# Kernel optimization log

Hardware: AMD Instinct MI355X
Metric: run time of the kernel (lower is better)

The kernel has to match this reference:

```python
import jax, jax.numpy as jnp
import numpy as np

NUM_NODES = 100000
NUM_EDGES = 1600000
NUM_GRAPHS = 64
D_IN = 128
HID = 256
N_ATTR = 8
D_OUT = 1


def setup_inputs() -> dict:
    key = jax.random.key(0)
    ks = jax.random.split(key, 16)
    x = jax.random.normal(ks[0], (NUM_NODES, D_IN), dtype=jnp.float32)
    edge_index = jax.random.randint(ks[1], (2, NUM_EDGES), 0, NUM_NODES, dtype=jnp.int64)
    batch = jnp.sort(jax.random.randint(ks[2], (NUM_NODES,), 0, NUM_GRAPHS, dtype=jnp.int64))
    graph_attr = jax.random.normal(ks[3], (NUM_GRAPHS, N_ATTR), dtype=jnp.float32)
    def lin(k, fi, fo):
        s = 1.0 / np.sqrt(fi)
        return jax.random.uniform(k, (fi, fo), jnp.float32, -s, s)
    # SAGEConv: lin_l (applied to aggregated neighbors, has bias) + lin_r (root, no bias)
    W1l = lin(ks[4], D_IN, HID); b1 = jnp.zeros((HID,), jnp.float32)
    W1r = lin(ks[5], D_IN, HID)
    W2l = lin(ks[6], HID, HID); b2 = jnp.zeros((HID,), jnp.float32)
    W2r = lin(ks[7], HID, HID)
    Wf1 = lin(ks[8], HID + N_ATTR, HID); bf1 = jnp.zeros((HID,), jnp.float32)
    Wf2 = lin(ks[9], HID, D_OUT); bf2 = jnp.zeros((D_OUT,), jnp.float32)
    return {"x": x, "edge_index": edge_index, "batch": batch, "graph_attr": graph_attr,
            "W1l": W1l, "b1": b1, "W1r": W1r, "W2l": W2l, "b2": b2, "W2r": W2r,
            "Wf1": Wf1, "bf1": bf1, "Wf2": Wf2, "bf2": bf2}


def _mean_agg(h, src, dst, num_segments):
    # gather source features, scatter-mean into destination nodes
    s = jax.ops.segment_sum(h[src], dst, num_segments=num_segments)
    cnt = jax.ops.segment_sum(jnp.ones((src.shape[0], 1), h.dtype), dst, num_segments=num_segments)
    return s / jnp.maximum(cnt, 1.0)


def _sage(h, src, dst, Wl, b, Wr):
    agg = _mean_agg(h, src, dst, h.shape[0])
    return agg @ Wl + b + h @ Wr


def reference(x, edge_index, batch, graph_attr, W1l, b1, W1r, W2l, b2, W2r, Wf1, bf1, Wf2, bf2):
    src, dst = edge_index[0], edge_index[1]
    h = jax.nn.relu(_sage(x, src, dst, W1l, b1, W1r))
    h = _sage(h, src, dst, W2l, b2, W2r)
    # global mean pool over graphs
    gsum = jax.ops.segment_sum(h, batch, num_segments=NUM_GRAPHS)
    gcnt = jax.ops.segment_sum(jnp.ones((h.shape[0], 1), h.dtype), batch, num_segments=NUM_GRAPHS)
    g = gsum / jnp.maximum(gcnt, 1.0)
    g = jnp.concatenate([g, graph_attr.reshape(-1, N_ATTR)], axis=1)
    g = jax.nn.relu(g @ Wf1 + bf1)
    return g @ Wf2 + bf2
```

## Files before the change

### kernel.cpp

```cpp
#include <hip/hip_runtime.h>
#include <stdint.h>

#define NN 100000
#define NE 1600000
#define NG 64
#define DIN 128
#define HID 256
#define NATTR 8
#define NBK 391
#define CAP 6144
#define PCH 4096
#define BWW 25000
#define CB 12756
#define AEL 2048

typedef unsigned short u16;
typedef __attribute__((ext_vector_type(8))) short s16x8;
typedef __attribute__((ext_vector_type(4))) float f32x4;
typedef __attribute__((ext_vector_type(2))) float f32x2;

__device__ __forceinline__ int imaxi(int a, int b) { return a > b ? a : b; }
__device__ __forceinline__ u16 f2bf(float f) {
    unsigned u = __float_as_uint(f);
    return (u16)((u + 0x7fffu + ((u >> 16) & 1u)) >> 16);
}
__device__ __forceinline__ void gload16(const void* g, void* l) {
    __builtin_amdgcn_global_load_lds((const __attribute__((address_space(1))) void*)g,
                                     (__attribute__((address_space(3))) void*)l, 16, 0, 0);
}


__global__ void k_prep(const float4* __restrict__ x4, ushort4* __restrict__ xb4,
                       const float* __restrict__ W1l, const float* __restrict__ W1r,
                       u16* __restrict__ W1lt, u16* __restrict__ W1rt,
                       float4* __restrict__ P84, const int* __restrict__ batch,
                       int* __restrict__ goff, int* __restrict__ gcnt,
                       int* __restrict__ cursor) {
    int b = blockIdx.x, t = threadIdx.x;
    if (b < CB) {
        int i = b * 256 + t;
        const int NX4 = NN * DIN / 4;
        if (i < NX4) {
            float4 v = x4[i];
            ushort4 o;
            o.x = f2bf(v.x); o.y = f2bf(v.y); o.z = f2bf(v.z); o.w = f2bf(v.w);
            xb4[i] = o;
        } else {
            int j = i - NX4;
            if (j < 32768) {
                int n = j >> 7, k = j & 127;
                W1lt[j] = f2bf(W1l[k * HID + n]);
            } else if (j < 65536) {
                int jj = j - 32768;
                int n = jj >> 7, k = jj & 127;
                W1rt[jj] = f2bf(W1r[k * HID + n]);
            }
        }
    } else if (b < CB + 256) {
        int i = (b - CB) * 256 + t;
        P84[i] = make_float4(0.f, 0.f, 0.f, 0.f);
    } else {
        for (int i = t; i < NBK; i += 256) cursor[i] = 0;
        int g = t;
        if (g <= NG) {
            int lo = 0, hi = NN;
            while (lo < hi) {
                int mid = (lo + hi) >> 1;
                if (batch[mid] < g) lo = mid + 1; else hi = mid;
            }
            goff[g] = lo;
        }
        __syncthreads();
        if (g < NG) gcnt[g] = goff[g + 1] - goff[g];
    }
}


__global__ __launch_bounds__(256) void k_part(const int* __restrict__ ei,
                                              int* __restrict__ cursor,
                                              unsigned* __restrict__ pairs) {
    __shared__ unsigned spk[PCH];
    __shared__ unsigned short sbk[PCH];
    __shared__ int hist[NBK], gb[NBK];
    __shared__ int sc[512];
    int t = threadIdx.x;
    int c0 = blockIdx.x * PCH;
    int n = NE - c0; if (n > PCH) n = PCH;
    for (int i = t; i < NBK; i += 256) hist[i] = 0;
    __syncthreads();
    unsigned mypk[16]; unsigned short mybk[16]; int myoff[16];
#pragma unroll
    for (int j = 0; j < 16; j++) {
        int i = t + j * 256;
        myoff[j] = -1;
        if (i < n) {
            int e = c0 + i;
            unsigned d = (unsigned)__builtin_nontemporal_load(&ei[NE + e]);
            unsigned s = (unsigned)__builtin_nontemporal_load(&ei[e]);
            unsigned bk = d >> 8;
            mypk[j] = ((d & 255u) << 24) | s;
            mybk[j] = (unsigned short)bk;
            myoff[j] = atomicAdd(&hist[bk], 1);
        }
    }
    __syncthreads();
    sc[t] = (t < NBK) ? hist[t] : 0;
    sc[t + 256] = (t + 256 < NBK) ? hist[t + 256] : 0;
    __syncthreads();
    for (int off = 1; off < 512; off <<= 1) {
        int v0 = (t >= off) ? sc[t - off] : 0;
        int v1 = (t + 256 >= off) ? sc[t + 256 - off] : 0;
        __syncthreads();
        sc[t] += v0; sc[t + 256] += v1;
        __syncthreads();
    }
    if (t < NBK && hist[t] > 0) gb[t] = atomicAdd(&cursor[t], hist[t]);
    if (t + 256 < NBK && hist[t + 256] > 0)
        gb[t + 256] = atomicAdd(&cursor[t + 256], hist[t + 256]);
    __syncthreads();
#pragma unroll
    for (int j = 0; j < 16; j++) {
        if (myoff[j] >= 0) {
            int bk = mybk[j];
            int pos = sc[bk] - hist[bk] + myoff[j];
            spk[pos] = mypk[j];
            sbk[pos] = (unsigned short)bk;
        }
    }
    __syncthreads();
    for (int i = t; i < n; i += 256) {
        int bk = sbk[i];
        int local = gb[bk] + (i - (sc[bk] - hist[bk]));
        pairs[(size_t)bk * CAP + local] = spk[i];
    }
}


__global__ __launch_bounds__(256) void k_csr(const unsigned* __restrict__ pairs,
                                             const int* __restrict__ cursor,
                                             int* __restrict__ rowptr,
                                             unsigned* __restrict__ col) {
    __shared__ unsigned colL[CAP];
    __shared__ int csc[512];
    __shared__ int cnt[256], cur[256], sc[256];
    int b = blockIdx.x, t = threadIdx.x;
    csc[t] = (t < NBK) ? cursor[t] : 0;
    csc[t + 256] = (t + 256 < NBK) ? cursor[t + 256] : 0;
    __syncthreads();
    for (int off = 1; off < 512; off <<= 1) {
        int v0 = (t >= off) ? csc[t - off] : 0;
        int v1 = (t + 256 >= off) ? csc[t + 256 - off] : 0;
        __syncthreads();
        csc[t] += v0; csc[t + 256] += v1;
        __syncthreads();
    }
    int obase = (b == 0) ? 0 : csc[b - 1];
    int ecnt = cursor[b];
    const unsigned* pp = pairs + (size_t)b * CAP;
    cnt[t] = 0;
    __syncthreads();
    for (int i = t; i < ecnt; i += 256)
        atomicAdd(&cnt[pp[i] >> 24], 1);
    __syncthreads();
    sc[t] = cnt[t];
    __syncthreads();
    for (int off = 1; off < 256; off <<= 1) {
        int v = (t >= off) ? sc[t - off] : 0;
        __syncthreads();
        sc[t] += v;
        __syncthreads();
    }
    int lr = sc[t] - cnt[t];
    cur[t] = lr;
    int node = (b << 8) + t;
    if (node < NN) rowptr[node] = obase + lr;
    if (b == NBK - 1 && t == 0) rowptr[NN] = obase + ecnt;
    __syncthreads();
    for (int i = t; i < ecnt; i += 256) {
        unsigned p = pp[i];
        int dl = p >> 24;
        int pos = atomicAdd(&cur[dl], 1);
        int dd = cnt[dl]; if (dd > 32767) dd = 32767;
        colL[pos] = ((unsigned)dd << 17) | (p & 0xFFFFFFu);
    }
    __syncthreads();
    for (int i = t; i < ecnt; i += 256)
        col[obase + i] = colL[i];
}


__global__ __launch_bounds__(256, 8) void k_agg(const uint4* __restrict__ xb4,
                                                uint4* __restrict__ agg4,
                                                const int* __restrict__ rowptr,
                                                const unsigned* __restrict__ col) {
    __shared__ unsigned scol[AEL];
    int t = threadIdx.x;
    int base = blockIdx.x * 16;
    int wave = t >> 6, lane = t & 63;
    int qtr = lane >> 4, li = lane & 15;
    int node = base + (wave << 2) + qtr;
    int s = rowptr[node], e = rowptr[node + 1];
    int bs = rowptr[base], be = rowptr[base + 16];
    int bn = be - bs;
    bool inl = bn <= AEL;
    if (inl)
        for (int j = t; j < bn; j += 256) scol[j] = col[bs + j];
    __syncthreads();

    f32x2 b01 = {0.f, 0.f}, b23 = {0.f, 0.f}, b45 = {0.f, 0.f}, b67 = {0.f, 0.f};
    const uint4* xp = xb4 + li;

#define ACC8(V) do { \
        f32x2 p; \
        p[0] = __uint_as_float((V).x << 16); p[1] = __uint_as_float((V).x & 0xffff0000u); b01 += p; \
        p[0] = __uint_as_float((V).y << 16); p[1] = __uint_as_float((V).y & 0xffff0000u); b23 += p; \
        p[0] = __uint_as_float((V).z << 16); p[1] = __uint_as_float((V).z & 0xffff0000u); b45 += p; \
        p[0] = __uint_as_float((V).w << 16); p[1] = __uint_as_float((V).w & 0xffff0000u); b67 += p; \
    } while (0)

#define CL(X) scol[(X) - bs]
#define CG(X) col[X]
#define AGG_BODY(CIDX) do { \
        for (; i + 8 <= e; i += 8) { \
            unsigned c0 = (CIDX(i + 0)) & 0x1FFFFu; \
            unsigned c1 = (CIDX(i + 1)) & 0x1FFFFu; \
            unsigned c2 = (CIDX(i + 2)) & 0x1FFFFu; \
            unsigned c3 = (CIDX(i + 3)) & 0x1FFFFu; \
            unsigned c4 = (CIDX(i + 4)) & 0x1FFFFu; \
            unsigned c5 = (CIDX(i + 5)) & 0x1FFFFu; \
            unsigned c6 = (CIDX(i + 6)) & 0x1FFFFu; \
            unsigned c7 = (CIDX(i + 7)) & 0x1FFFFu; \
            uint4 w0 = xp[(size_t)c0 * 16]; \
            uint4 w1 = xp[(size_t)c1 * 16]; \
            uint4 w2 = xp[(size_t)c2 * 16]; \
            uint4 w3 = xp[(size_t)c3 * 16]; \
            uint4 w4 = xp[(size_t)c4 * 16]; \
            uint4 w5 = xp[(size_t)c5 * 16]; \
            uint4 w6 = xp[(size_t)c6 * 16]; \
            uint4 w7 = xp[(size_t)c7 * 16]; \
            ACC8(w0); ACC8(w1); ACC8(w2); ACC8(w3); \
            ACC8(w4); ACC8(w5); ACC8(w6); ACC8(w7); \
        } \
        for (; i + 2 <= e; i += 2) { \
            unsigned c0 = (CIDX(i + 0)) & 0x1FFFFu; \
            unsigned c1 = (CIDX(i + 1)) & 0x1FFFFu; \
            uint4 w0 = xp[(size_t)c0 * 16]; \
            uint4 w1 = xp[(size_t)c1 * 16]; \
            ACC8(w0); ACC8(w1); \
        } \
        if (i < e) { \
            unsigned c0 = (CIDX(i)) & 0x1FFFFu; \
            uint4 w0 = xp[(size_t)c0 * 16]; \
            ACC8(w0); \
        } \
    } while (0)

    int i = s;
    if (inl) { AGG_BODY(CL); } else { AGG_BODY(CG); }
#undef AGG_BODY
#undef CL
#undef CG
#undef ACC8

    float inv = 1.f / (float)imaxi(e - s, 1);
    uint4 o;
    o.x = (((unsigned)f2bf(b01[1] * inv)) << 16) | (unsigned)f2bf(b01[0] * inv);
    o.y = (((unsigned)f2bf(b23[1] * inv)) << 16) | (unsigned)f2bf(b23[0] * inv);
    o.z = (((unsigned)f2bf(b45[1] * inv)) << 16) | (unsigned)f2bf(b45[0] * inv);
    o.w = (((unsigned)f2bf(b67[1] * inv)) << 16) | (unsigned)f2bf(b67[0] * inv);
    agg4[(size_t)node * 16 + li] = o;
}


__global__ __launch_bounds__(512) void k_gemm1(
    const u16* __restrict__ agg1, const u16* __restrict__ xb,
    const u16* __restrict__ W1lt, const u16* __restrict__ W1rt,
    const float* __restrict__ b1, u16* __restrict__ h1t) {
    __shared__ u16 As[128][32];
    __shared__ u16 Bs[256][32];
    int t = threadIdx.x;
    int m0 = blockIdx.x * 128;
    int wave = t >> 6, lane = t & 63;
    int wm = wave & 1, wn = wave >> 1;
    int lm = lane & 15, quad = lane >> 4;
    int ar = t >> 2, aq = t & 3;
    f32x4 acc[4][4] = {};
    const u16* Ap = agg1;
    const u16* Bp = W1lt;
#pragma unroll
    for (int ph = 0; ph < 2; ph++) {
        for (int k0 = 0; k0 < DIN; k0 += 32) {
            gload16(Ap + (size_t)(m0 + ar) * DIN + k0 + aq * 8, &As[wave * 16][0]);
#pragma unroll
            for (int i = 0; i < 2; i++) {
                int r = (t + i * 512) >> 2;
                gload16(Bp + (size_t)r * DIN + k0 + aq * 8, &Bs[wave * 16 + i * 128][0]);
            }
            __syncthreads();
            s16x8 af[4], bfr[4];
#pragma unroll
            for (int i = 0; i < 4; i++) {
                af[i]  = *(const s16x8*)&As[wm * 64 + i * 16 + lm][quad * 8];
                bfr[i] = *(const s16x8*)&Bs[wn * 64 + i * 16 + lm][quad * 8];
            }
#pragma unroll
            for (int mi = 0; mi < 4; mi++)
#pragma unroll
                for (int ni = 0; ni < 4; ni++)
                    acc[mi][ni] = __builtin_amdgcn_mfma_f32_16x16x32_bf16(
                        af[mi], bfr[ni], acc[mi][ni], 0, 0, 0);
            __syncthreads();
        }
        Ap = xb; Bp = W1rt;
    }
#pragma unroll
    for (int ni = 0; ni < 4; ni++) {
        int colf = wn * 64 + ni * 16 + lm;
        float bias = b1[colf];
#pragma unroll
        for (int mi = 0; mi < 4; mi++) {
            int row = m0 + wm * 64 + mi * 16 + quad * 4;
            if (row < NN) {
                ushort4 o;
                o.x = f2bf(fmaxf(acc[mi][ni][0] + bias, 0.f));
                o.y = f2bf(fmaxf(acc[mi][ni][1] + bias, 0.f));
                o.z = f2bf(fmaxf(acc[mi][ni][2] + bias, 0.f));
                o.w = f2bf(fmaxf(acc[mi][ni][3] + bias, 0.f));
                *(ushort4*)(h1t + (size_t)colf * NN + row) = o;
            }
        }
    }
}


__global__ __launch_bounds__(256) void k_bw(
    const int* __restrict__ rowptr, const unsigned* __restrict__ col,
    const int* __restrict__ goff, u16* __restrict__ Wbt) {
    int b = blockIdx.x, t = threadIdx.x;
    if (b < 256) {
        __shared__ float bins[BWW];
        int g = b >> 2, w = b & 3;
        int lo = w * BWW;
        for (int i = t; i < BWW; i += 256) bins[i] = 0.f;
        __syncthreads();
        int ebeg = rowptr[goff[g]], eend = rowptr[goff[g + 1]];
        for (int i = ebeg + t; i < eend; i += 256) {
            unsigned c = col[i];
            unsigned sl = (c & 0x1FFFFu) - lo;
            if (sl < (unsigned)BWW) atomicAdd(&bins[sl], 1.0f / (float)(c >> 17));
        }
        __syncthreads();
        u16* out = Wbt + (size_t)g * NN + lo;
        for (int k = t; k < BWW / 4; k += 256) {
            ushort4 o;
            o.x = f2bf(bins[4 * k + 0]); o.y = f2bf(bins[4 * k + 1]);
            o.z = f2bf(bins[4 * k + 2]); o.w = f2bf(bins[4 * k + 3]);
            *(ushort4*)(out + 4 * k) = o;
        }
    } else {
        int g = b - 256;
        int a = goff[g], bnd = goff[g + 1];
        u16* out = Wbt + (size_t)(NG + g) * NN;
        for (int k = t; k < NN / 4; k += 256) {
            int c0 = 4 * k;
            ushort4 o;
            o.x = (c0 + 0 >= a && c0 + 0 < bnd) ? 0x3F80 : 0;
            o.y = (c0 + 1 >= a && c0 + 1 < bnd) ? 0x3F80 : 0;
            o.z = (c0 + 2 >= a && c0 + 2 < bnd) ? 0x3F80 : 0;
            o.w = (c0 + 3 >= a && c0 + 3 < bnd) ? 0x3F80 : 0;
            *(ushort4*)(out + c0) = o;
        }
    }
}


#define KCHUNK 512

__global__ __launch_bounds__(512) void k_poolg(
    const u16* __restrict__ Wbt, const u16* __restrict__ h1t, float* __restrict__ P8) {
    __shared__ u16 As[128][32];
    __shared__ u16 Bs[256][32];
    int t = threadIdx.x;
    int kbase = blockIdx.x * KCHUNK;
    int krem = NN - kbase;
    int ksteps = (krem < KCHUNK ? krem : KCHUNK) >> 5;
    int wave = t >> 6, lane = t & 63;
    int wm = wave & 1, wn = wave >> 1;
    int lm = lane & 15, quad = lane >> 4;
    int ar = t >> 2, aq = t & 3;
    float* P = P8 + (size_t)(blockIdx.x & 7) * 128 * HID;
    f32x4 acc[4][4] = {};
    for (int ks = 0; ks < ksteps; ks++) {
        int k0 = kbase + ks * 32;
        gload16(Wbt + (size_t)ar * NN + k0 + aq * 8, &As[wave * 16][0]);
#pragma unroll
        for (int i = 0; i < 2; i++) {
            int r = (t + i * 512) >> 2;
            gload16(h1t + (size_t)r * NN + k0 + aq * 8, &Bs[wave * 16 + i * 128][0]);
        }
        __syncthreads();
        s16x8 af[4], bfr[4];
#pragma unroll
        for (int i = 0; i < 4; i++) {
            af[i]  = *(const s16x8*)&As[wm * 64 + i * 16 + lm][quad * 8];
            bfr[i] = *(const s16x8*)&Bs[wn * 64 + i * 16 + lm][quad * 8];
        }
#pragma unroll
        for (int mi = 0; mi < 4; mi++)
#pragma unroll
            for (int ni = 0; ni < 4; ni++)
                acc[mi][ni] = __builtin_amdgcn_mfma_f32_16x16x32_bf16(
                    af[mi], bfr[ni], acc[mi][ni], 0, 0, 0);
        __syncthreads();
    }
#pragma unroll
    for (int mi = 0; mi < 4; mi++)
#pragma unroll
        for (int ni = 0; ni < 4; ni++) {
            int gcol = wm * 64 + mi * 16 + quad * 4;
            int feat = wn * 64 + ni * 16 + lm;
#pragma unroll
            for (int r = 0; r < 4; r++)
                atomicAdd(&P[(gcol + r) * HID + feat], acc[mi][ni][r]);
        }
}


__global__ void k_head(const float* __restrict__ P8, const int* __restrict__ gcnt,
                       const float* __restrict__ gattr,
                       const float* __restrict__ W2l, const float* __restrict__ b2,
                       const float* __restrict__ W2r,
                       const float* __restrict__ Wf1, const float* __restrict__ bf1,
                       const float* __restrict__ Wf2, const float* __restrict__ bf2v,
                       float* __restrict__ out) {
    __shared__ float pa[HID], ph[HID], gv[HID + NATTR];
    __shared__ float red[256];
    int g = blockIdx.x, t = threadIdx.x;
    float sa = 0.f, sh = 0.f;
#pragma unroll
    for (int c = 0; c < 8; c++) {
        sa += P8[(size_t)c * 128 * HID + g * HID + t];
        sh += P8[(size_t)c * 128 * HID + (NG + g) * HID + t];
    }
    pa[t] = sa; ph[t] = sh;
    __syncthreads();
    float s = 0.f;
    for (int k = 0; k < HID; k++)
        s += pa[k] * W2l[k * HID + t] + ph[k] * W2r[k * HID + t];
    float invc = 1.f / (float)imaxi(gcnt[g], 1);
    gv[t] = s * invc + b2[t];
    if (t < NATTR) gv[HID + t] = gattr[g * NATTR + t];
    __syncthreads();
    float h = bf1[t];
    for (int k = 0; k < HID + NATTR; k++) h += gv[k] * Wf1[k * HID + t];
    h = fmaxf(h, 0.f);
    red[t] = h * Wf2[t];
    __syncthreads();
    for (int off = 128; off > 0; off >>= 1) {
        if (t < off) red[t] += red[t + off];
        __syncthreads();
    }
    if (t == 0) out[g] = red[0] + bf2v[0];
}


extern "C" void kernel_launch(void* const* d_in, const int* in_sizes, int n_in,
                              void* d_out, int out_size, void* d_ws, size_t ws_size,
                              hipStream_t stream) {
    (void)in_sizes; (void)n_in; (void)out_size; (void)ws_size;
    const float* x     = (const float*)d_in[0];
    const int*   ei    = (const int*)d_in[1];
    const int*   batch = (const int*)d_in[2];
    const float* gattr = (const float*)d_in[3];
    const float* W1l   = (const float*)d_in[4];
    const float* b1    = (const float*)d_in[5];
    const float* W1r   = (const float*)d_in[6];
    const float* W2l   = (const float*)d_in[7];
    const float* b2    = (const float*)d_in[8];
    const float* W2r   = (const float*)d_in[9];
    const float* Wf1   = (const float*)d_in[10];
    const float* bf1   = (const float*)d_in[11];
    const float* Wf2   = (const float*)d_in[12];
    const float* bf2v  = (const float*)d_in[13];
    float* out = (float*)d_out;

    uint8_t* w = (uint8_t*)d_ws;
    size_t off = 0;
    auto alloc = [&](size_t bytes) -> void* {
        void* p = w + off;
        off += (bytes + 255) & ~(size_t)255;
        return p;
    };
    u16*      xb     = (u16*)alloc((size_t)NN * DIN * 2);
    u16*      agg1   = (u16*)alloc((size_t)NN * DIN * 2);
    u16*      h1t    = (u16*)alloc((size_t)NN * HID * 2);
    u16*      Wbt    = (u16*)alloc((size_t)128 * NN * 2);
    u16*      W1lt   = (u16*)alloc((size_t)HID * DIN * 2);
    u16*      W1rt   = (u16*)alloc((size_t)HID * DIN * 2);
    unsigned* pairs  = (unsigned*)alloc((size_t)NBK * CAP * 4);
    int*      rowptr = (int*)alloc((size_t)(NN + 1) * 4);
    unsigned* col    = (unsigned*)alloc((size_t)NE * 4);
    int*      cursor = (int*)alloc((NBK + 1) * 4);
    int*      goff   = (int*)alloc((NG + 1) * 4);
    int*      gcnt   = (int*)alloc(NG * 4);
    float*    P8     = (float*)alloc((size_t)8 * 128 * HID * 4);

    k_prep<<<CB + 257, 256, 0, stream>>>((const float4*)x, (ushort4*)xb, W1l, W1r,
                                         W1lt, W1rt, (float4*)P8, batch, goff, gcnt,
                                         cursor);

    k_part<<<(NE + PCH - 1) / PCH, 256, 0, stream>>>(ei, cursor, pairs);
    k_csr<<<NBK, 256, 0, stream>>>(pairs, cursor, rowptr, col);

    k_agg<<<NN / 16, 256, 0, stream>>>((const uint4*)xb, (uint4*)agg1, rowptr, col);
    k_gemm1<<<(NN + 127) / 128, 512, 0, stream>>>(agg1, xb, W1lt, W1rt, b1, h1t);

    k_bw<<<320, 256, 0, stream>>>(rowptr, col, goff, Wbt);
    k_poolg<<<(NN + KCHUNK - 1) / KCHUNK, 512, 0, stream>>>(Wbt, h1t, P8);

    k_head<<<NG, 256, 0, stream>>>(P8, gcnt, gattr, W2l, b2, W2r, Wf1, bf1, Wf2, bf2v, out);
}
```

Measured before the change: 364.2 us.

## Split head kernel K-loops across two thread halves and tune aggregation scheduling

The head kernel now runs 512 threads per graph. Each half handles half of the partial-sum chunks and half of each matrix-vector reduction, and the two halves are combined through shared memory, which shortens the serial per-thread loops. The aggregation kernel lowers its occupancy hint from 8 to 4 waves per SIMD, giving the compiler more registers. It also adds a scheduling barrier so all eight gathers are issued before any accumulation. The gains could be offset by the extra syncs in the head and by less latency hiding in the aggregation.

Result: slower. 380.6 us (+4.5%).

```diff
diff --git a/kernel.cpp b/kernel.cpp
--- a/kernel.cpp
+++ b/kernel.cpp
@@ -189,7 +189,7 @@
 }
 
 
-__global__ __launch_bounds__(256, 8) void k_agg(const uint4* __restrict__ xb4,
+__global__ __launch_bounds__(256, 4) void k_agg(const uint4* __restrict__ xb4,
                                                 uint4* __restrict__ agg4,
                                                 const int* __restrict__ rowptr,
                                                 const unsigned* __restrict__ col) {
@@ -238,6 +238,7 @@
             uint4 w5 = xp[(size_t)c5 * 16]; \
             uint4 w6 = xp[(size_t)c6 * 16]; \
             uint4 w7 = xp[(size_t)c7 * 16]; \
+            __builtin_amdgcn_sched_barrier(0); \
             ACC8(w0); ACC8(w1); ACC8(w2); ACC8(w3); \
             ACC8(w4); ACC8(w5); ACC8(w6); ACC8(w7); \
         } \
@@ -426,35 +427,56 @@
 }
 
 
-__global__ void k_head(const float* __restrict__ P8, const int* __restrict__ gcnt,
-                       const float* __restrict__ gattr,
-                       const float* __restrict__ W2l, const float* __restrict__ b2,
-                       const float* __restrict__ W2r,
-                       const float* __restrict__ Wf1, const float* __restrict__ bf1,
-                       const float* __restrict__ Wf2, const float* __restrict__ bf2v,
-                       float* __restrict__ out) {
+__global__ __launch_bounds__(512) void k_head(
+    const float* __restrict__ P8, const int* __restrict__ gcnt,
+    const float* __restrict__ gattr,
+    const float* __restrict__ W2l, const float* __restrict__ b2,
+    const float* __restrict__ W2r,
+    const float* __restrict__ Wf1, const float* __restrict__ bf1,
+    const float* __restrict__ Wf2, const float* __restrict__ bf2v,
+    float* __restrict__ out) {
     __shared__ float pa[HID], ph[HID], gv[HID + NATTR];
+    __shared__ float paP[2][HID], phP[2][HID];
+    __shared__ float red2[512];
     __shared__ float red[256];
     int g = blockIdx.x, t = threadIdx.x;
+    int f = t & 255, h = t >> 8;
     float sa = 0.f, sh = 0.f;
 #pragma unroll
-    for (int c = 0; c < 8; c++) {
-        sa += P8[(size_t)c * 128 * HID + g * HID + t];
-        sh += P8[(size_t)c * 128 * HID + (NG + g) * HID + t];
-    }
-    pa[t] = sa; ph[t] = sh;
+    for (int c = 0; c < 4; c++) {
+        int cc = h * 4 + c;
+        sa += P8[(size_t)cc * 128 * HID + g * HID + f];
+        sh += P8[(size_t)cc * 128 * HID + (NG + g) * HID + f];
+    }
+    paP[h][f] = sa; phP[h][f] = sh;
+    __syncthreads();
+    if (h == 0) {
+        pa[f] = paP[0][f] + paP[1][f];
+        ph[f] = phP[0][f] + phP[1][f];
+    }
     __syncthreads();
     float s = 0.f;
-    for (int k = 0; k < HID; k++)
-        s += pa[k] * W2l[k * HID + t] + ph[k] * W2r[k * HID + t];
-    float invc = 1.f / (float)imaxi(gcnt[g], 1);
-    gv[t] = s * invc + b2[t];
-    if (t < NATTR) gv[HID + t] = gattr[g * NATTR + t];
-    __syncthreads();
-    float h = bf1[t];
-    for (int k = 0; k < HID + NATTR; k++) h += gv[k] * Wf1[k * HID + t];
-    h = fmaxf(h, 0.f);
-    red[t] = h * Wf2[t];
+    for (int k = h * 128; k < h * 128 + 128; k++)
+        s += pa[k] * W2l[k * HID + f] + ph[k] * W2r[k * HID + f];
+    red2[t] = s;
+    __syncthreads();
+    if (h == 0) {
+        float sfull = red2[f] + red2[f + 256];
+        float invc = 1.f / (float)imaxi(gcnt[g], 1);
+        gv[f] = sfull * invc + b2[f];
+        if (f < NATTR) gv[HID + f] = gattr[g * NATTR + f];
+    }
+    __syncthreads();
+    float hsum = 0.f;
+    for (int k = h * 132; k < h * 132 + 132; k++)
+        hsum += gv[k] * Wf1[k * HID + f];
+    red2[t] = hsum;
+    __syncthreads();
+    if (h == 0) {
+        float hv = red2[f] + red2[f + 256] + bf1[f];
+        hv = fmaxf(hv, 0.f);
+        red[f] = hv * Wf2[f];
+    }
     __syncthreads();
     for (int off = 128; off > 0; off >>= 1) {
         if (t < off) red[t] += red[t + off];
@@ -518,5 +540,5 @@
     k_bw<<<320, 256, 0, stream>>>(rowptr, col, goff, Wbt);
     k_poolg<<<(NN + KCHUNK - 1) / KCHUNK, 512, 0, stream>>>(Wbt, h1t, P8);
 
-    k_head<<<NG, 256, 0, stream>>>(P8, gcnt, gattr, W2l, b2, W2r, Wf1, bf1, Wf2, bf2v, out);
-}
+    k_head<<<NG, 512, 0, stream>>>(P8, gcnt, gattr, W2l, b2, W2r, Wf1, bf1, Wf2, bf2v, out);
+}
```
